# Performance work log

Measured on AMD Instinct MI355X. Metric: run time of the kernel, lower is better.

The kernel has to match this reference:

```python
import jax, jax.numpy as jnp
import numpy as np

B, T, E, H = 2, 4096, 768, 12
D = E // H  # head_dim = 64


def setup_inputs() -> dict:
    key = jax.random.key(0)
    ks = jax.random.split(key, 9)
    s = 1.0 / np.sqrt(E)
    return {
        "x": jax.random.normal(ks[0], (B, T, E), dtype=jnp.float32),
        "wq": jax.random.normal(ks[1], (E, E), dtype=jnp.float32) * s,
        "bq": jnp.zeros((E,), dtype=jnp.float32),
        "wk": jax.random.normal(ks[2], (E, E), dtype=jnp.float32) * s,
        "bk": jnp.zeros((E,), dtype=jnp.float32),
        "wv": jax.random.normal(ks[3], (E, E), dtype=jnp.float32) * s,
        "bv": jnp.zeros((E,), dtype=jnp.float32),
        "wo": jax.random.normal(ks[4], (E, E), dtype=jnp.float32) * s,
        "bo": jnp.zeros((E,), dtype=jnp.float32),
    }


def reference(x, wq, bq, wk, bk, wv, bv, wo, bo):
    # Linear projections (torch Linear: x @ W.T + b; weights here stored as (in,out))
    q = x @ wq + bq  # (B,T,E)
    k = x @ wk + bk
    v = x @ wv + bv

    def split(t):
        return t.reshape(B, T, H, D).transpose(0, 2, 1, 3)  # (B,H,T,D)

    q, k, v = split(q), split(k), split(v)
    scale = 1.0 / np.sqrt(D).astype(np.float32)
    scores = jnp.einsum("bhtd,bhsd->bhts", q, k) * scale  # (B,H,T,T)
    causal = jnp.tril(jnp.ones((T, T), dtype=bool))
    scores = jnp.where(causal, scores, -jnp.inf)
    attn = jax.nn.softmax(scores, axis=-1)
    out = jnp.einsum("bhts,bhsd->bhtd", attn, v)  # (B,H,T,D)
    out = out.transpose(0, 2, 1, 3).reshape(B, T, E)
    return out @ wo + bo
```

## Files before the change

### kernel.cpp

```cpp
#include <hip/hip_runtime.h>
#include <hip/hip_bf16.h>

#define TSEQ 4096
#define EMB 768
#define NH 12
#define DH 64
#define BT 8192

typedef __attribute__((ext_vector_type(8))) short bf16x8;
typedef __attribute__((ext_vector_type(4))) float f32x4;

#define FENCE() asm volatile("" ::: "memory")

__device__ __forceinline__ f32x4 mfma16(bf16x8 a, bf16x8 b, f32x4 c) {
    return __builtin_amdgcn_mfma_f32_16x16x32_bf16(a, b, c, 0, 0, 0);
}

__device__ __forceinline__ void gload16(const void* g, void* l) {
    __builtin_amdgcn_global_load_lds((const __attribute__((address_space(1))) void*)g,
                                     (__attribute__((address_space(3))) void*)l, 16, 0, 0);
}

__global__ __launch_bounds__(256) void conv_x_k(const float* __restrict__ x,
                                                __hip_bfloat16* __restrict__ xb) {
    int i = (blockIdx.x * 256 + threadIdx.x) * 4;
    float4 v = *(const float4*)(x + i);
    union { unsigned short u[4]; uint2 p; } o;
    __hip_bfloat16 t0 = __float2bfloat16(v.x); o.u[0] = *(unsigned short*)&t0;
    __hip_bfloat16 t1 = __float2bfloat16(v.y); o.u[1] = *(unsigned short*)&t1;
    __hip_bfloat16 t2 = __float2bfloat16(v.z); o.u[2] = *(unsigned short*)&t2;
    __hip_bfloat16 t3 = __float2bfloat16(v.w); o.u[3] = *(unsigned short*)&t3;
    *(uint2*)(xb + i) = o.p;
}

__global__ __launch_bounds__(256) void conv_w_k(const float* w0, const float* w1,
                                                const float* w2, const float* w3,
                                                __hip_bfloat16* o0, __hip_bfloat16* o1,
                                                __hip_bfloat16* o2, __hip_bfloat16* o3) {
    const float* w; __hip_bfloat16* o;
    switch (blockIdx.z) {
        case 0: w = w0; o = o0; break;
        case 1: w = w1; o = o1; break;
        case 2: w = w2; o = o2; break;
        default: w = w3; o = o3; break;
    }
    __shared__ float tile[32][33];
    int tx = threadIdx.x & 31, ty = threadIdx.x >> 5;
    int kb = blockIdx.y * 32, nb = blockIdx.x * 32;
    for (int i = 0; i < 32; i += 8)
        tile[ty + i][tx] = w[(size_t)(kb + ty + i) * EMB + nb + tx];
    __syncthreads();
    for (int i = 0; i < 32; i += 8)
        o[(size_t)(nb + ty + i) * EMB + kb + tx] = __float2bfloat16(tile[tx][ty + i]);
}

__device__ __forceinline__ void gemm_body(const __hip_bfloat16* __restrict__ A,
                                          const __hip_bfloat16* __restrict__ Wt,
                                          const float* __restrict__ bias,
                                          void* __restrict__ outp, int mode, float scale) {
    __shared__ alignas(16) char As[2][8192];
    __shared__ alignas(16) char Bs[2][8192];
    const int m0 = blockIdx.x * 128, n0 = blockIdx.y * 128;
    const int tid = threadIdx.x;
    const int lane = tid & 63, l15 = lane & 15, lg = lane >> 4;
    const int wave = tid >> 6, wm = wave >> 1, wn = wave & 1;
    const int swz = (l15 & 7) << 4;

    int mrow_[2]; int kelem_[2];
#pragma unroll
    for (int c = 0; c < 2; ++c) {
        int p = c * 4096 + tid * 16;
        int lrow = p >> 7, w = p & 127;
        int wp = w ^ ((lrow & 7) << 4);
        mrow_[c] = lrow + ((wp >> 6) & 1) * 64;
        kelem_[c] = (wp & 63) >> 1;
    }

    f32x4 acc[4][4];
    for (int i = 0; i < 4; ++i)
        for (int j = 0; j < 4; ++j) acc[i][j] = (f32x4){0.f, 0.f, 0.f, 0.f};

    auto stage = [&](int buf, int k0) {
#pragma unroll
        for (int c = 0; c < 2; ++c)
            gload16(A + (size_t)(m0 + mrow_[c]) * EMB + k0 + kelem_[c],
                    As[buf] + c * 4096 + wave * 1024);
#pragma unroll
        for (int c = 0; c < 2; ++c)
            gload16(Wt + (size_t)(n0 + mrow_[c]) * EMB + k0 + kelem_[c],
                    Bs[buf] + c * 4096 + wave * 1024);
    };

    stage(0, 0);
    const int NK = EMB / 32;
    for (int ks = 0; ks < NK; ++ks) {
        const int cur = ks & 1;
        const bool pre = (ks + 1 < NK);
        if (pre) stage(cur ^ 1, (ks + 1) * 32);
        if (pre) asm volatile("s_waitcnt vmcnt(4)" ::: "memory");
        else     asm volatile("s_waitcnt vmcnt(0)" ::: "memory");
        FENCE(); __builtin_amdgcn_s_barrier(); FENCE();
        bf16x8 af[4], bfv[4];
#pragma unroll
        for (int f = 0; f < 4; ++f)
            af[f] = *(const bf16x8*)(As[cur] + (f * 16 + l15) * 128 + ((wm * 64 + lg * 16) ^ swz));
#pragma unroll
        for (int f = 0; f < 4; ++f)
            bfv[f] = *(const bf16x8*)(Bs[cur] + (f * 16 + l15) * 128 + ((wn * 64 + lg * 16) ^ swz));
        __builtin_amdgcn_s_setprio(1);
#pragma unroll
        for (int i = 0; i < 4; ++i)
#pragma unroll
            for (int j = 0; j < 4; ++j)
                acc[i][j] = mfma16(af[i], bfv[j], acc[i][j]);
        __builtin_amdgcn_s_setprio(0);
        FENCE(); __builtin_amdgcn_s_barrier(); FENCE();
    }

#pragma unroll
    for (int i = 0; i < 4; ++i) {
#pragma unroll
        for (int j = 0; j < 4; ++j) {
            const int n = n0 + wn * 64 + j * 16 + l15;
            const float bv = bias[n];
            const int mbase = m0 + wm * 64 + i * 16 + lg * 4;
#pragma unroll
            for (int r = 0; r < 4; ++r) {
                const int m = mbase + r;
                const float val = (acc[i][j][r] + bv) * scale;
                if (mode == 2) {
                    ((float*)outp)[(size_t)m * EMB + n] = val;
                } else {
                    const int b = m >> 12, t = m & (TSEQ - 1);
                    const int h = n >> 6, d = n & 63;
                    size_t addr;
                    if (mode == 0) addr = ((size_t)(b * NH + h) * TSEQ + t) * DH + d;
                    else           addr = ((size_t)(b * NH + h) * DH + d) * TSEQ + t;
                    ((__hip_bfloat16*)outp)[addr] = __float2bfloat16(val);
                }
            }
        }
    }
}

__global__ __launch_bounds__(256) void qkv_k(const __hip_bfloat16* __restrict__ xb,
                                             const __hip_bfloat16* __restrict__ wqT,
                                             const __hip_bfloat16* __restrict__ wkT,
                                             const __hip_bfloat16* __restrict__ wvT,
                                             const float* __restrict__ bq,
                                             const float* __restrict__ bk,
                                             const float* __restrict__ bv,
                                             __hip_bfloat16* __restrict__ qo,
                                             __hip_bfloat16* __restrict__ ko,
                                             __hip_bfloat16* __restrict__ vo) {
    const __hip_bfloat16* Wt; const float* bias; void* o; int mode; float scale;
    const float cq = 0.125f * 1.44269504089f;
    switch (blockIdx.z) {
        case 0:  Wt = wqT; bias = bq; o = qo; mode = 0; scale = cq;  break;
        case 1:  Wt = wkT; bias = bk; o = ko; mode = 0; scale = 1.f; break;
        default: Wt = wvT; bias = bv; o = vo; mode = 1; scale = 1.f; break;
    }
    gemm_body(xb, Wt, bias, o, mode, scale);
}

__global__ __launch_bounds__(256) void oproj_k(const __hip_bfloat16* __restrict__ abf,
                                               const __hip_bfloat16* __restrict__ woT,
                                               const float* __restrict__ bo,
                                               float* __restrict__ out) {
    gemm_body(abf, woT, bo, out, 2, 1.f);
}

__global__ __launch_bounds__(256) void attn_k(const __hip_bfloat16* __restrict__ qb,
                                              const __hip_bfloat16* __restrict__ kb,
                                              const __hip_bfloat16* __restrict__ vt,
                                              __hip_bfloat16* __restrict__ ab) {
    __shared__ alignas(16) char Ks[2][8192];
    __shared__ alignas(16) char Vs[2][8192];
    __shared__ alignas(16) char pbuf[4][2048];
    const int lane = threadIdx.x & 63, l15 = lane & 15, lg = lane >> 4;
    const int wave = threadIdx.x >> 6;
    const int bid = blockIdx.x;
    const int xcd = bid & 7, slot = bid >> 3;
    const int pair = slot & 31, hgrp = slot >> 5;
    const int bh = xcd + hgrp * 8;
    const __hip_bfloat16* Qh = qb + (size_t)bh * TSEQ * DH;
    const __hip_bfloat16* Kh = kb + (size_t)bh * TSEQ * DH;
    const __hip_bfloat16* Vh = vt + (size_t)bh * DH * TSEQ;
    char* Pb = pbuf[wave];
    const int swz = (l15 & 7) << 4;
    const int b = bh / NH, h = bh % NH;

    bf16x8 ones8;
#pragma unroll
    for (int j = 0; j < 8; ++j) ones8[j] = (short)0x3F80;

    unsigned ka[8];
#pragma unroll
    for (int st = 0; st < 4; ++st)
#pragma unroll
        for (int ks = 0; ks < 2; ++ks)
            ka[st * 2 + ks] = (unsigned)((st * 16 + l15) * 128 + ((ks * 64 + lg * 16) ^ swz));
    char* pw[4]; char* pr[2];
#pragma unroll
    for (int st = 0; st < 4; ++st) pw[st] = Pb + l15 * 128 + ((st * 32 + lg * 8) ^ swz);
#pragma unroll
    for (int ks = 0; ks < 2; ++ks) pr[ks] = Pb + l15 * 128 + ((ks * 64 + lg * 16) ^ swz);
    const int dthr = wave * 16 + l15 - lg * 4;

    int r_[2], wp_[2];
#pragma unroll
    for (int c = 0; c < 2; ++c) {
        int p = c * 4096 + wave * 1024 + lane * 16;
        int r = p >> 7, w = p & 127;
        r_[c] = r;
        wp_[c] = (w ^ ((r & 7) << 4)) >> 1;
    }

#define SBODY(BUF, PRE, MASKB) do {                                              \
    if (PRE) {                                                                   \
        gload16(kg0, Ks[(BUF) ^ 1] + wave * 1024);                               \
        gload16(kg1, Ks[(BUF) ^ 1] + 4096 + wave * 1024);                        \
        gload16(vg0, Vs[(BUF) ^ 1] + wave * 1024);                               \
        gload16(vg1, Vs[(BUF) ^ 1] + 4096 + wave * 1024);                        \
        kg0 += 8192; kg1 += 8192; vg0 += 128; vg1 += 128;                        \
        asm volatile("s_waitcnt vmcnt(4)" ::: "memory");                         \
    } else {                                                                     \
        asm volatile("s_waitcnt vmcnt(0)" ::: "memory");                         \
    }                                                                            \
    FENCE(); __builtin_amdgcn_s_barrier(); FENCE();                              \
    f32x4 sa[4];                                                                 \
    __builtin_amdgcn_s_setprio(1);                                               \
    _Pragma("unroll")                                                            \
    for (int st = 0; st < 4; ++st) {                                             \
        f32x4 z = (f32x4){0.f, 0.f, 0.f, 0.f};                                   \
        z = mfma16(*(const bf16x8*)(Ks[BUF] + ka[st * 2 + 0]), qf0, z);          \
        z = mfma16(*(const bf16x8*)(Ks[BUF] + ka[st * 2 + 1]), qf1, z);          \
        sa[st] = z;                                                              \
    }                                                                            \
    __builtin_amdgcn_s_setprio(0);                                               \
    if (MASKB) {                                                                 \
        _Pragma("unroll")                                                        \
        for (int st = 0; st < 4; ++st)                                           \
            _Pragma("unroll")                                                    \
            for (int r = 0; r < 4; ++r)                                          \
                if (st * 16 + r > dthr) sa[st][r] = -INFINITY;                   \
    }                                                                            \
    float mx = fmaxf(fmaxf(sa[0][0], sa[0][1]), sa[0][2]);                       \
    mx = fmaxf(fmaxf(mx, sa[0][3]), sa[1][0]);                                   \
    mx = fmaxf(fmaxf(mx, sa[1][1]), sa[1][2]);                                   \
    mx = fmaxf(fmaxf(mx, sa[1][3]), sa[2][0]);                                   \
    mx = fmaxf(fmaxf(mx, sa[2][1]), sa[2][2]);                                   \
    mx = fmaxf(fmaxf(mx, sa[2][3]), sa[3][0]);                                   \
    mx = fmaxf(fmaxf(mx, sa[3][1]), sa[3][2]);                                   \
    mx = fmaxf(mx, sa[3][3]);                                                    \
    mx = fmaxf(mx, __shfl_xor(mx, 16));                                          \
    mx = fmaxf(mx, __shfl_xor(mx, 32));                                          \
    float mnew = m;                                                              \
    if (!__all(mx <= m + 8.0f)) {                                                \
        mnew = fmaxf(m, mx);                                                     \
        const float rs = exp2f(m - mnew);                                        \
        m = mnew;                                                                \
        float fr[4];                                                             \
        _Pragma("unroll")                                                        \
        for (int r = 0; r < 4; ++r) fr[r] = __shfl(rs, lg * 4 + r);              \
        _Pragma("unroll")                                                        \
        for (int dt = 0; dt < 4; ++dt) {                                         \
            f32x4 ov = o[dt];                                                    \
            _Pragma("unroll")                                                    \
            for (int r = 0; r < 4; ++r) ov[r] *= fr[r];                          \
            o[dt] = ov;                                                          \
        }                                                                        \
        _Pragma("unroll")                                                        \
        for (int r = 0; r < 4; ++r) lacc[r] *= fr[r];                            \
    }                                                                            \
    _Pragma("unroll")                                                            \
    for (int st = 0; st < 4; ++st) {                                             \
        union { unsigned short u[4]; uint2 v; } pk;                              \
        _Pragma("unroll")                                                        \
        for (int r = 0; r < 4; ++r) {                                            \
            const float p = exp2f(sa[st][r] - mnew);                             \
            __hip_bfloat16 hb = __float2bfloat16(p);                             \
            pk.u[r] = *(unsigned short*)&hb;                                     \
        }                                                                        \
        *(uint2*)pw[st] = pk.v;                                                  \
    }                                                                            \
    asm volatile("s_waitcnt lgkmcnt(0)" ::: "memory");                           \
    __builtin_amdgcn_s_setprio(1);                                               \
    bf16x8 pf0 = *(const bf16x8*)pr[0];                                          \
    bf16x8 pf1 = *(const bf16x8*)pr[1];                                          \
    lacc = mfma16(pf0, ones8, lacc);                                             \
    lacc = mfma16(pf1, ones8, lacc);                                             \
    _Pragma("unroll")                                                            \
    for (int dt = 0; dt < 4; ++dt)                                               \
        o[dt] = mfma16(pf0, *(const bf16x8*)(Vs[BUF] + ka[dt * 2 + 0]), o[dt]);  \
    _Pragma("unroll")                                                            \
    for (int dt = 0; dt < 4; ++dt)                                               \
        o[dt] = mfma16(pf1, *(const bf16x8*)(Vs[BUF] + ka[dt * 2 + 1]), o[dt]);  \
    __builtin_amdgcn_s_setprio(0);                                               \
    asm volatile("s_waitcnt lgkmcnt(0)" ::: "memory");                           \
    FENCE(); __builtin_amdgcn_s_barrier(); FENCE();                              \
} while (0)

    for (int tt = 0; tt < 2; ++tt) {
        const int tile = tt ? (63 - pair) : pair;
        const int q0 = tile * 64 + wave * 16;

        bf16x8 qf0 = *(const bf16x8*)(Qh + (size_t)(q0 + l15) * DH + lg * 8);
        bf16x8 qf1 = *(const bf16x8*)(Qh + (size_t)(q0 + l15) * DH + 32 + lg * 8);

        f32x4 o[4];
#pragma unroll
        for (int dt = 0; dt < 4; ++dt) o[dt] = (f32x4){0.f, 0.f, 0.f, 0.f};
        f32x4 lacc = (f32x4){0.f, 0.f, 0.f, 0.f};
        float m = -1e30f;

        const char* kg0 = (const char*)(Kh + (size_t)r_[0] * DH + wp_[0]);
        const char* kg1 = (const char*)(Kh + (size_t)r_[1] * DH + wp_[1]);
        const char* vg0 = (const char*)(Vh + (size_t)r_[0] * TSEQ + wp_[0]);
        const char* vg1 = (const char*)(Vh + (size_t)r_[1] * TSEQ + wp_[1]);

        const int nsb = tile + 1;
        gload16(kg0, Ks[0] + wave * 1024);
        gload16(kg1, Ks[0] + 4096 + wave * 1024);
        gload16(vg0, Vs[0] + wave * 1024);
        gload16(vg1, Vs[0] + 4096 + wave * 1024);
        kg0 += 8192; kg1 += 8192; vg0 += 128; vg1 += 128;

        int sb = 0;
        while (sb + 2 <= nsb) {
            SBODY(0, true, false);
            SBODY(1, (sb + 2 < nsb), (sb + 1 == nsb - 1));
            sb += 2;
        }
        if (sb < nsb) SBODY(0, false, true);

        float inv[4];
#pragma unroll
        for (int r = 0; r < 4; ++r) inv[r] = 1.0f / lacc[r];
#pragma unroll
        for (int r = 0; r < 4; ++r) {
            const int qrow = q0 + lg * 4 + r;
            const size_t rowbase = ((size_t)b * TSEQ + qrow) * EMB + h * DH;
#pragma unroll
            for (int dt = 0; dt < 4; ++dt)
                ab[rowbase + dt * 16 + l15] = __float2bfloat16(o[dt][r] * inv[r]);
        }
    }
#undef SBODY
}

extern "C" void kernel_launch(void* const* d_in, const int* in_sizes, int n_in,
                              void* d_out, int out_size, void* d_ws, size_t ws_size,
                              hipStream_t stream) {
    (void)in_sizes; (void)n_in; (void)out_size; (void)ws_size;
    const float* x  = (const float*)d_in[0];
    const float* wq = (const float*)d_in[1];
    const float* bq = (const float*)d_in[2];
    const float* wk = (const float*)d_in[3];
    const float* bk = (const float*)d_in[4];
    const float* wv = (const float*)d_in[5];
    const float* bv = (const float*)d_in[6];
    const float* wo = (const float*)d_in[7];
    const float* bo = (const float*)d_in[8];
    float* out = (float*)d_out;

    char* ws = (char*)d_ws;
    size_t off = 0;
    auto alloc = [&](size_t bytes) {
        char* p = ws + off;
        off += (bytes + 255) & ~(size_t)255;
        return p;
    };
    __hip_bfloat16* xb  = (__hip_bfloat16*)alloc((size_t)BT * EMB * 2);
    __hip_bfloat16* qbf = (__hip_bfloat16*)alloc((size_t)BT * EMB * 2);
    __hip_bfloat16* kbf = (__hip_bfloat16*)alloc((size_t)BT * EMB * 2);
    __hip_bfloat16* vtb = (__hip_bfloat16*)alloc((size_t)BT * EMB * 2);
    __hip_bfloat16* abf = (__hip_bfloat16*)alloc((size_t)BT * EMB * 2);
    __hip_bfloat16* wqT = (__hip_bfloat16*)alloc((size_t)EMB * EMB * 2);
    __hip_bfloat16* wkT = (__hip_bfloat16*)alloc((size_t)EMB * EMB * 2);
    __hip_bfloat16* wvT = (__hip_bfloat16*)alloc((size_t)EMB * EMB * 2);
    __hip_bfloat16* woT = (__hip_bfloat16*)alloc((size_t)EMB * EMB * 2);

    conv_x_k<<<BT * EMB / 1024, 256, 0, stream>>>(x, xb);
    conv_w_k<<<dim3(24, 24, 4), 256, 0, stream>>>(wq, wk, wv, wo, wqT, wkT, wvT, woT);
    qkv_k<<<dim3(64, 6, 3), 256, 0, stream>>>(xb, wqT, wkT, wvT, bq, bk, bv, qbf, kbf, vtb);
    attn_k<<<768, 256, 0, stream>>>(qbf, kbf, vtb, abf);
    oproj_k<<<dim3(64, 6), 256, 0, stream>>>(abf, woT, bo, out);
}
```

Before: 207.8 us.

## Share K/V tiles between paired causal query tiles in one pass

The attention kernel previously handled its low and high query tiles one after the other, streaming K/V from global memory twice. Now both tiles run in a single pass over K/V: each staged K/V block feeds the high tile and, while still in range, the low tile, so the low tile's global loads are dropped. The load pipeline is reordered so the prefetch is issued after the barrier with a full vmcnt(0) wait, and launch bounds ask for 3 blocks per CU. The cost is higher register pressure from keeping two sets of accumulators and Q fragments, which the occupancy hint may turn into spills. The pipelining is also weaker, since the wait and barrier now come before the prefetch of the next block.

```diff
diff --git a/kernel.cpp b/kernel.cpp
--- a/kernel.cpp
+++ b/kernel.cpp
@@ -170,10 +170,10 @@
     gemm_body(abf, woT, bo, out, 2, 1.f);
 }
 
-__global__ __launch_bounds__(256) void attn_k(const __hip_bfloat16* __restrict__ qb,
-                                              const __hip_bfloat16* __restrict__ kb,
-                                              const __hip_bfloat16* __restrict__ vt,
-                                              __hip_bfloat16* __restrict__ ab) {
+__global__ __launch_bounds__(256, 3) void attn_k(const __hip_bfloat16* __restrict__ qb,
+                                                 const __hip_bfloat16* __restrict__ kb,
+                                                 const __hip_bfloat16* __restrict__ vt,
+                                                 __hip_bfloat16* __restrict__ ab) {
     __shared__ alignas(16) char Ks[2][8192];
     __shared__ alignas(16) char Vs[2][8192];
     __shared__ alignas(16) char pbuf[4][2048];
@@ -216,25 +216,43 @@
         wp_[c] = (w ^ ((r & 7) << 4)) >> 1;
     }
 
-#define SBODY(BUF, PRE, MASKB) do {                                              \
-    if (PRE) {                                                                   \
-        gload16(kg0, Ks[(BUF) ^ 1] + wave * 1024);                               \
-        gload16(kg1, Ks[(BUF) ^ 1] + 4096 + wave * 1024);                        \
-        gload16(vg0, Vs[(BUF) ^ 1] + wave * 1024);                               \
-        gload16(vg1, Vs[(BUF) ^ 1] + 4096 + wave * 1024);                        \
-        kg0 += 8192; kg1 += 8192; vg0 += 128; vg1 += 128;                        \
-        asm volatile("s_waitcnt vmcnt(4)" ::: "memory");                         \
-    } else {                                                                     \
-        asm volatile("s_waitcnt vmcnt(0)" ::: "memory");                         \
-    }                                                                            \
-    FENCE(); __builtin_amdgcn_s_barrier(); FENCE();                              \
+    const int lo = pair, hi = 63 - pair;
+    const int q0l = lo * 64 + wave * 16;
+    const int q0h = hi * 64 + wave * 16;
+    const int nsb = hi + 1;
+
+    bf16x8 qh0 = *(const bf16x8*)(Qh + (size_t)(q0h + l15) * DH + lg * 8);
+    bf16x8 qh1 = *(const bf16x8*)(Qh + (size_t)(q0h + l15) * DH + 32 + lg * 8);
+    bf16x8 ql0 = *(const bf16x8*)(Qh + (size_t)(q0l + l15) * DH + lg * 8);
+    bf16x8 ql1 = *(const bf16x8*)(Qh + (size_t)(q0l + l15) * DH + 32 + lg * 8);
+
+    f32x4 oh[4], ol[4];
+#pragma unroll
+    for (int dt = 0; dt < 4; ++dt) { oh[dt] = (f32x4){0.f,0.f,0.f,0.f}; ol[dt] = (f32x4){0.f,0.f,0.f,0.f}; }
+    f32x4 lh = (f32x4){0.f,0.f,0.f,0.f}, ll = (f32x4){0.f,0.f,0.f,0.f};
+    float mh = -1e30f, ml = -1e30f;
+
+    const char* kg0 = (const char*)(Kh + (size_t)r_[0] * DH + wp_[0]);
+    const char* kg1 = (const char*)(Kh + (size_t)r_[1] * DH + wp_[1]);
+    const char* vg0 = (const char*)(Vh + (size_t)r_[0] * TSEQ + wp_[0]);
+    const char* vg1 = (const char*)(Vh + (size_t)r_[1] * TSEQ + wp_[1]);
+
+#define STAGE(DST) do {                                                          \
+    gload16(kg0, Ks[DST] + wave * 1024);                                         \
+    gload16(kg1, Ks[DST] + 4096 + wave * 1024);                                  \
+    gload16(vg0, Vs[DST] + wave * 1024);                                         \
+    gload16(vg1, Vs[DST] + 4096 + wave * 1024);                                  \
+    kg0 += 8192; kg1 += 8192; vg0 += 128; vg1 += 128;                            \
+} while (0)
+
+#define TUNIT(BUF, Q0, Q1, OV, LA, MM, MASKB) do {                               \
     f32x4 sa[4];                                                                 \
     __builtin_amdgcn_s_setprio(1);                                               \
     _Pragma("unroll")                                                            \
     for (int st = 0; st < 4; ++st) {                                             \
         f32x4 z = (f32x4){0.f, 0.f, 0.f, 0.f};                                   \
-        z = mfma16(*(const bf16x8*)(Ks[BUF] + ka[st * 2 + 0]), qf0, z);          \
-        z = mfma16(*(const bf16x8*)(Ks[BUF] + ka[st * 2 + 1]), qf1, z);          \
+        z = mfma16(*(const bf16x8*)(Ks[BUF] + ka[st * 2 + 0]), Q0, z);           \
+        z = mfma16(*(const bf16x8*)(Ks[BUF] + ka[st * 2 + 1]), Q1, z);           \
         sa[st] = z;                                                              \
     }                                                                            \
     __builtin_amdgcn_s_setprio(0);                                               \
@@ -255,23 +273,23 @@
     mx = fmaxf(mx, sa[3][3]);                                                    \
     mx = fmaxf(mx, __shfl_xor(mx, 16));                                          \
     mx = fmaxf(mx, __shfl_xor(mx, 32));                                          \
-    float mnew = m;                                                              \
-    if (!__all(mx <= m + 8.0f)) {                                                \
-        mnew = fmaxf(m, mx);                                                     \
-        const float rs = exp2f(m - mnew);                                        \
-        m = mnew;                                                                \
+    float mnew = MM;                                                             \
+    if (!__all(mx <= MM + 8.0f)) {                                               \
+        mnew = fmaxf(MM, mx);                                                    \
+        const float rs = exp2f(MM - mnew);                                       \
+        MM = mnew;                                                               \
         float fr[4];                                                             \
         _Pragma("unroll")                                                        \
         for (int r = 0; r < 4; ++r) fr[r] = __shfl(rs, lg * 4 + r);              \
         _Pragma("unroll")                                                        \
         for (int dt = 0; dt < 4; ++dt) {                                         \
-            f32x4 ov = o[dt];                                                    \
+            f32x4 ov = OV[dt];                                                   \
             _Pragma("unroll")                                                    \
             for (int r = 0; r < 4; ++r) ov[r] *= fr[r];                          \
-            o[dt] = ov;                                                          \
+            OV[dt] = ov;                                                         \
         }                                                                        \
         _Pragma("unroll")                                                        \
-        for (int r = 0; r < 4; ++r) lacc[r] *= fr[r];                            \
+        for (int r = 0; r < 4; ++r) LA[r] *= fr[r];                              \
     }                                                                            \
     _Pragma("unroll")                                                            \
     for (int st = 0; st < 4; ++st) {                                             \
@@ -285,68 +303,67 @@
         *(uint2*)pw[st] = pk.v;                                                  \
     }                                                                            \
     asm volatile("s_waitcnt lgkmcnt(0)" ::: "memory");                           \
-    __builtin_amdgcn_s_setprio(1);                                               \
     bf16x8 pf0 = *(const bf16x8*)pr[0];                                          \
     bf16x8 pf1 = *(const bf16x8*)pr[1];                                          \
-    lacc = mfma16(pf0, ones8, lacc);                                             \
-    lacc = mfma16(pf1, ones8, lacc);                                             \
+    __builtin_amdgcn_s_setprio(1);                                               \
+    LA = mfma16(pf0, ones8, LA);                                                 \
+    LA = mfma16(pf1, ones8, LA);                                                 \
     _Pragma("unroll")                                                            \
     for (int dt = 0; dt < 4; ++dt)                                               \
-        o[dt] = mfma16(pf0, *(const bf16x8*)(Vs[BUF] + ka[dt * 2 + 0]), o[dt]);  \
+        OV[dt] = mfma16(pf0, *(const bf16x8*)(Vs[BUF] + ka[dt * 2 + 0]), OV[dt]);\
     _Pragma("unroll")                                                            \
     for (int dt = 0; dt < 4; ++dt)                                               \
-        o[dt] = mfma16(pf1, *(const bf16x8*)(Vs[BUF] + ka[dt * 2 + 1]), o[dt]);  \
+        OV[dt] = mfma16(pf1, *(const bf16x8*)(Vs[BUF] + ka[dt * 2 + 1]), OV[dt]);\
     __builtin_amdgcn_s_setprio(0);                                               \
-    asm volatile("s_waitcnt lgkmcnt(0)" ::: "memory");                           \
+} while (0)
+
+#define SBODY(BUF, PRE, LOACT, MHI, MLO) do {                                    \
+    asm volatile("s_waitcnt vmcnt(0)" ::: "memory");                             \
     FENCE(); __builtin_amdgcn_s_barrier(); FENCE();                              \
+    if (PRE) STAGE((BUF) ^ 1);                                                   \
+    TUNIT(BUF, qh0, qh1, oh, lh, mh, MHI);                                       \
+    if (LOACT) TUNIT(BUF, ql0, ql1, ol, ll, ml, MLO);                            \
 } while (0)
 
-    for (int tt = 0; tt < 2; ++tt) {
-        const int tile = tt ? (63 - pair) : pair;
-        const int q0 = tile * 64 + wave * 16;
-
-        bf16x8 qf0 = *(const bf16x8*)(Qh + (size_t)(q0 + l15) * DH + lg * 8);
-        bf16x8 qf1 = *(const bf16x8*)(Qh + (size_t)(q0 + l15) * DH + 32 + lg * 8);
-
-        f32x4 o[4];
-#pragma unroll
-        for (int dt = 0; dt < 4; ++dt) o[dt] = (f32x4){0.f, 0.f, 0.f, 0.f};
-        f32x4 lacc = (f32x4){0.f, 0.f, 0.f, 0.f};
-        float m = -1e30f;
-
-        const char* kg0 = (const char*)(Kh + (size_t)r_[0] * DH + wp_[0]);
-        const char* kg1 = (const char*)(Kh + (size_t)r_[1] * DH + wp_[1]);
-        const char* vg0 = (const char*)(Vh + (size_t)r_[0] * TSEQ + wp_[0]);
-        const char* vg1 = (const char*)(Vh + (size_t)r_[1] * TSEQ + wp_[1]);
-
-        const int nsb = tile + 1;
-        gload16(kg0, Ks[0] + wave * 1024);
-        gload16(kg1, Ks[0] + 4096 + wave * 1024);
-        gload16(vg0, Vs[0] + wave * 1024);
-        gload16(vg1, Vs[0] + 4096 + wave * 1024);
-        kg0 += 8192; kg1 += 8192; vg0 += 128; vg1 += 128;
-
-        int sb = 0;
-        while (sb + 2 <= nsb) {
-            SBODY(0, true, false);
-            SBODY(1, (sb + 2 < nsb), (sb + 1 == nsb - 1));
-            sb += 2;
+    STAGE(0);
+    int sb = 0;
+    while (sb + 2 <= nsb) {
+        SBODY(0, true, sb <= lo, false, sb == lo);
+        SBODY(1, sb + 2 < nsb, sb + 1 <= lo, sb + 1 == nsb - 1, sb + 1 == lo);
+        sb += 2;
+    }
+    if (sb < nsb) SBODY(0, false, sb <= lo, true, sb == lo);
+
+#undef SBODY
+#undef TUNIT
+#undef STAGE
+
+    {
+        float inv[4];
+#pragma unroll
+        for (int r = 0; r < 4; ++r) inv[r] = 1.0f / lh[r];
+#pragma unroll
+        for (int r = 0; r < 4; ++r) {
+            const int qrow = q0h + lg * 4 + r;
+            const size_t rowbase = ((size_t)b * TSEQ + qrow) * EMB + h * DH;
+#pragma unroll
+            for (int dt = 0; dt < 4; ++dt)
+                ab[rowbase + dt * 16 + l15] = __float2bfloat16(oh[dt][r] * inv[r]);
         }
-        if (sb < nsb) SBODY(0, false, true);
-
+    }
+    {
         float inv[4];
 #pragma unroll
-        for (int r = 0; r < 4; ++r) inv[r] = 1.0f / lacc[r];
+        for (int r = 0; r < 4; ++r) inv[r] = 1.0f / ll[r];
 #pragma unroll
         for (int r = 0; r < 4; ++r) {
-            const int qrow = q0 + lg * 4 + r;
+            const int qrow = q0l + lg * 4 + r;
             const size_t rowbase = ((size_t)b * TSEQ + qrow) * EMB + h * DH;
 #pragma unroll
             for (int dt = 0; dt < 4; ++dt)
-                ab[rowbase + dt * 16 + l15] = __float2bfloat16(o[dt][r] * inv[r]);
+                ab[rowbase + dt * 16 + l15] = __float2bfloat16(ol[dt][r] * inv[r]);
         }
     }
-#undef SBODY
 }
 
 extern "C" void kernel_launch(void* const* d_in, const int* in_sizes, int n_in,
```

Measured after the change: 198.9 us. 1.04x faster.

## Rework causal attention to 32x32 MFMA tiles with register-resident P

Applied to the files above, without the earlier changes.

Rewrites the attention kernel so each wave handles 32 query rows with 32x32x16 bf16 MFMAs instead of 16x16x32. The softmax probabilities are exchanged between half-waves with lane shuffles rather than written to and re-read from an LDS staging buffer, which removes that buffer and its waits. Each block now processes one 128-row query tile, ordered largest first, instead of a balanced pair of 64-row tiles. The staging wait becomes a full vmcnt(0) before the barrier, which may reduce load/compute overlap, and the larger accumulators raise register pressure.

```diff
diff --git a/kernel.cpp b/kernel.cpp
--- a/kernel.cpp
+++ b/kernel.cpp
@@ -9,11 +9,21 @@
 
 typedef __attribute__((ext_vector_type(8))) short bf16x8;
 typedef __attribute__((ext_vector_type(4))) float f32x4;
+typedef __attribute__((ext_vector_type(16))) float f32x16;
 
 #define FENCE() asm volatile("" ::: "memory")
 
 __device__ __forceinline__ f32x4 mfma16(bf16x8 a, bf16x8 b, f32x4 c) {
     return __builtin_amdgcn_mfma_f32_16x16x32_bf16(a, b, c, 0, 0, 0);
+}
+__device__ __forceinline__ f32x16 mfma32(bf16x8 a, bf16x8 b, f32x16 c) {
+    return __builtin_amdgcn_mfma_f32_32x32x16_bf16(a, b, c, 0, 0, 0);
+}
+__device__ __forceinline__ f32x16 zero16() {
+    f32x16 z;
+#pragma unroll
+    for (int i = 0; i < 16; ++i) z[i] = 0.f;
+    return z;
 }
 
 __device__ __forceinline__ void gload16(const void* g, void* l) {
@@ -176,36 +186,28 @@
                                               __hip_bfloat16* __restrict__ ab) {
     __shared__ alignas(16) char Ks[2][8192];
     __shared__ alignas(16) char Vs[2][8192];
-    __shared__ alignas(16) char pbuf[4][2048];
-    const int lane = threadIdx.x & 63, l15 = lane & 15, lg = lane >> 4;
+    const int lane = threadIdx.x & 63;
+    const int l31 = lane & 31, hiL = lane >> 5;
     const int wave = threadIdx.x >> 6;
     const int bid = blockIdx.x;
     const int xcd = bid & 7, slot = bid >> 3;
-    const int pair = slot & 31, hgrp = slot >> 5;
+    const int t = 31 - (slot & 31);
+    const int hgrp = slot >> 5;
     const int bh = xcd + hgrp * 8;
     const __hip_bfloat16* Qh = qb + (size_t)bh * TSEQ * DH;
     const __hip_bfloat16* Kh = kb + (size_t)bh * TSEQ * DH;
     const __hip_bfloat16* Vh = vt + (size_t)bh * DH * TSEQ;
-    char* Pb = pbuf[wave];
-    const int swz = (l15 & 7) << 4;
     const int b = bh / NH, h = bh % NH;
 
     bf16x8 ones8;
 #pragma unroll
     for (int j = 0; j < 8; ++j) ones8[j] = (short)0x3F80;
 
-    unsigned ka[8];
-#pragma unroll
-    for (int st = 0; st < 4; ++st)
-#pragma unroll
-        for (int ks = 0; ks < 2; ++ks)
-            ka[st * 2 + ks] = (unsigned)((st * 16 + l15) * 128 + ((ks * 64 + lg * 16) ^ swz));
-    char* pw[4]; char* pr[2];
-#pragma unroll
-    for (int st = 0; st < 4; ++st) pw[st] = Pb + l15 * 128 + ((st * 32 + lg * 8) ^ swz);
-#pragma unroll
-    for (int ks = 0; ks < 2; ++ks) pr[ks] = Pb + l15 * 128 + ((ks * 64 + lg * 16) ^ swz);
-    const int dthr = wave * 16 + l15 - lg * 4;
+    const int swzb = (l31 & 7) << 4;
+    int colx[4];
+#pragma unroll
+    for (int c = 0; c < 4; ++c) colx[c] = (c * 32 + hiL * 16) ^ swzb;
+    const int rb0 = l31 * 128, rb1 = (32 + l31) * 128;
 
     int r_[2], wp_[2];
 #pragma unroll
@@ -216,137 +218,137 @@
         wp_[c] = (w ^ ((r & 7) << 4)) >> 1;
     }
 
-#define SBODY(BUF, PRE, MASKB) do {                                              \
-    if (PRE) {                                                                   \
-        gload16(kg0, Ks[(BUF) ^ 1] + wave * 1024);                               \
-        gload16(kg1, Ks[(BUF) ^ 1] + 4096 + wave * 1024);                        \
-        gload16(vg0, Vs[(BUF) ^ 1] + wave * 1024);                               \
-        gload16(vg1, Vs[(BUF) ^ 1] + 4096 + wave * 1024);                        \
-        kg0 += 8192; kg1 += 8192; vg0 += 128; vg1 += 128;                        \
-        asm volatile("s_waitcnt vmcnt(4)" ::: "memory");                         \
-    } else {                                                                     \
-        asm volatile("s_waitcnt vmcnt(0)" ::: "memory");                         \
-    }                                                                            \
-    FENCE(); __builtin_amdgcn_s_barrier(); FENCE();                              \
-    f32x4 sa[4];                                                                 \
+    const int q0w = t * 128 + wave * 32;
+    const int nsb = 2 * t + 2;
+    const int sbd = (q0w + 31) >> 6;
+    const int dthrh = (q0w - 64 * sbd) + l31 - 4 * hiL;
+
+    const __hip_bfloat16* qrow = Qh + (size_t)(q0w + l31) * DH;
+    bf16x8 qf[4];
+#pragma unroll
+    for (int kd = 0; kd < 4; ++kd)
+        qf[kd] = *(const bf16x8*)(qrow + kd * 16 + hiL * 8);
+
+    f32x16 o0 = zero16(), o1 = zero16(), lacc = zero16();
+    float m = -1e30f;
+
+    const char* kg0 = (const char*)(Kh + (size_t)r_[0] * DH + wp_[0]);
+    const char* kg1 = (const char*)(Kh + (size_t)r_[1] * DH + wp_[1]);
+    const char* vg0 = (const char*)(Vh + (size_t)r_[0] * TSEQ + wp_[0]);
+    const char* vg1 = (const char*)(Vh + (size_t)r_[1] * TSEQ + wp_[1]);
+
+#define STAGE(DST) do {                                                          \
+    gload16(kg0, Ks[DST] + wave * 1024);                                         \
+    gload16(kg1, Ks[DST] + 4096 + wave * 1024);                                  \
+    gload16(vg0, Vs[DST] + wave * 1024);                                         \
+    gload16(vg1, Vs[DST] + 4096 + wave * 1024);                                  \
+    kg0 += 8192; kg1 += 8192; vg0 += 128; vg1 += 128;                            \
+} while (0)
+
+#define TUNIT(BUF, MASKB) do {                                                   \
+    f32x16 a0 = zero16(), a1 = zero16();                                         \
     __builtin_amdgcn_s_setprio(1);                                               \
     _Pragma("unroll")                                                            \
-    for (int st = 0; st < 4; ++st) {                                             \
-        f32x4 z = (f32x4){0.f, 0.f, 0.f, 0.f};                                   \
-        z = mfma16(*(const bf16x8*)(Ks[BUF] + ka[st * 2 + 0]), qf0, z);          \
-        z = mfma16(*(const bf16x8*)(Ks[BUF] + ka[st * 2 + 1]), qf1, z);          \
-        sa[st] = z;                                                              \
+    for (int kd = 0; kd < 4; ++kd) {                                             \
+        a0 = mfma32(*(const bf16x8*)(Ks[BUF] + rb0 + colx[kd]), qf[kd], a0);     \
+        a1 = mfma32(*(const bf16x8*)(Ks[BUF] + rb1 + colx[kd]), qf[kd], a1);     \
     }                                                                            \
     __builtin_amdgcn_s_setprio(0);                                               \
     if (MASKB) {                                                                 \
         _Pragma("unroll")                                                        \
-        for (int st = 0; st < 4; ++st)                                           \
-            _Pragma("unroll")                                                    \
-            for (int r = 0; r < 4; ++r)                                          \
-                if (st * 16 + r > dthr) sa[st][r] = -INFINITY;                   \
-    }                                                                            \
-    float mx = fmaxf(fmaxf(sa[0][0], sa[0][1]), sa[0][2]);                       \
-    mx = fmaxf(fmaxf(mx, sa[0][3]), sa[1][0]);                                   \
-    mx = fmaxf(fmaxf(mx, sa[1][1]), sa[1][2]);                                   \
-    mx = fmaxf(fmaxf(mx, sa[1][3]), sa[2][0]);                                   \
-    mx = fmaxf(fmaxf(mx, sa[2][1]), sa[2][2]);                                   \
-    mx = fmaxf(fmaxf(mx, sa[2][3]), sa[3][0]);                                   \
-    mx = fmaxf(fmaxf(mx, sa[3][1]), sa[3][2]);                                   \
-    mx = fmaxf(mx, sa[3][3]);                                                    \
-    mx = fmaxf(mx, __shfl_xor(mx, 16));                                          \
+        for (int r = 0; r < 16; ++r) {                                           \
+            if ((r & 3) + 8 * (r >> 2) > dthrh) a0[r] = -INFINITY;               \
+            if (32 + (r & 3) + 8 * (r >> 2) > dthrh) a1[r] = -INFINITY;          \
+        }                                                                        \
+    }                                                                            \
+    float mx = a0[0];                                                            \
+    _Pragma("unroll")                                                            \
+    for (int r = 1; r < 16; ++r) mx = fmaxf(mx, a0[r]);                          \
+    _Pragma("unroll")                                                            \
+    for (int r = 0; r < 16; ++r) mx = fmaxf(mx, a1[r]);                          \
     mx = fmaxf(mx, __shfl_xor(mx, 32));                                          \
     float mnew = m;                                                              \
     if (!__all(mx <= m + 8.0f)) {                                                \
         mnew = fmaxf(m, mx);                                                     \
         const float rs = exp2f(m - mnew);                                        \
         m = mnew;                                                                \
-        float fr[4];                                                             \
         _Pragma("unroll")                                                        \
-        for (int r = 0; r < 4; ++r) fr[r] = __shfl(rs, lg * 4 + r);              \
+        for (int r = 0; r < 16; ++r) {                                           \
+            const float fr = __shfl(rs, (r & 3) + 8 * (r >> 2) + 4 * hiL);       \
+            lacc[r] *= fr; o0[r] *= fr; o1[r] *= fr;                             \
+        }                                                                        \
+    }                                                                            \
+    _Pragma("unroll")                                                            \
+    for (int r = 0; r < 16; ++r) {                                               \
+        a0[r] = exp2f(a0[r] - mnew);                                             \
+        a1[r] = exp2f(a1[r] - mnew);                                             \
+    }                                                                            \
+    unsigned uu[2][4][2];                                                        \
+    _Pragma("unroll")                                                            \
+    for (int rg = 0; rg < 4; ++rg) {                                             \
+        asm("v_cvt_pk_bf16_f32 %0, %1, %2" : "=v"(uu[0][rg][0]) : "v"(a0[4*rg+0]), "v"(a0[4*rg+1])); \
+        asm("v_cvt_pk_bf16_f32 %0, %1, %2" : "=v"(uu[0][rg][1]) : "v"(a0[4*rg+2]), "v"(a0[4*rg+3])); \
+        asm("v_cvt_pk_bf16_f32 %0, %1, %2" : "=v"(uu[1][rg][0]) : "v"(a1[4*rg+0]), "v"(a1[4*rg+1])); \
+        asm("v_cvt_pk_bf16_f32 %0, %1, %2" : "=v"(uu[1][rg][1]) : "v"(a1[4*rg+2]), "v"(a1[4*rg+3])); \
+    }                                                                            \
+    unsigned px[2][4][2];                                                        \
+    _Pragma("unroll")                                                            \
+    for (int sp = 0; sp < 2; ++sp)                                               \
         _Pragma("unroll")                                                        \
-        for (int dt = 0; dt < 4; ++dt) {                                         \
-            f32x4 ov = o[dt];                                                    \
-            _Pragma("unroll")                                                    \
-            for (int r = 0; r < 4; ++r) ov[r] *= fr[r];                          \
-            o[dt] = ov;                                                          \
+        for (int rg = 0; rg < 4; ++rg) {                                         \
+            px[sp][rg][0] = __shfl_xor(uu[sp][rg][0], 32);                       \
+            px[sp][rg][1] = __shfl_xor(uu[sp][rg][1], 32);                       \
         }                                                                        \
-        _Pragma("unroll")                                                        \
-        for (int r = 0; r < 4; ++r) lacc[r] *= fr[r];                            \
-    }                                                                            \
-    _Pragma("unroll")                                                            \
-    for (int st = 0; st < 4; ++st) {                                             \
-        union { unsigned short u[4]; uint2 v; } pk;                              \
-        _Pragma("unroll")                                                        \
-        for (int r = 0; r < 4; ++r) {                                            \
-            const float p = exp2f(sa[st][r] - mnew);                             \
-            __hip_bfloat16 hb = __float2bfloat16(p);                             \
-            pk.u[r] = *(unsigned short*)&hb;                                     \
-        }                                                                        \
-        *(uint2*)pw[st] = pk.v;                                                  \
-    }                                                                            \
-    asm volatile("s_waitcnt lgkmcnt(0)" ::: "memory");                           \
+    bf16x8 pf[4];                                                                \
+    _Pragma("unroll")                                                            \
+    for (int c = 0; c < 4; ++c) {                                                \
+        const int sp = c >> 1, rgp = (c & 1) * 2;                                \
+        union { unsigned w[4]; bf16x8 v; } pk_;                                  \
+        pk_.w[0] = hiL ? px[sp][rgp + 1][0] : uu[sp][rgp][0];                    \
+        pk_.w[1] = hiL ? px[sp][rgp + 1][1] : uu[sp][rgp][1];                    \
+        pk_.w[2] = hiL ? uu[sp][rgp + 1][0] : px[sp][rgp][0];                    \
+        pk_.w[3] = hiL ? uu[sp][rgp + 1][1] : px[sp][rgp][1];                    \
+        pf[c] = pk_.v;                                                           \
+    }                                                                            \
     __builtin_amdgcn_s_setprio(1);                                               \
-    bf16x8 pf0 = *(const bf16x8*)pr[0];                                          \
-    bf16x8 pf1 = *(const bf16x8*)pr[1];                                          \
-    lacc = mfma16(pf0, ones8, lacc);                                             \
-    lacc = mfma16(pf1, ones8, lacc);                                             \
-    _Pragma("unroll")                                                            \
-    for (int dt = 0; dt < 4; ++dt)                                               \
-        o[dt] = mfma16(pf0, *(const bf16x8*)(Vs[BUF] + ka[dt * 2 + 0]), o[dt]);  \
-    _Pragma("unroll")                                                            \
-    for (int dt = 0; dt < 4; ++dt)                                               \
-        o[dt] = mfma16(pf1, *(const bf16x8*)(Vs[BUF] + ka[dt * 2 + 1]), o[dt]);  \
+    _Pragma("unroll")                                                            \
+    for (int c = 0; c < 4; ++c) lacc = mfma32(pf[c], ones8, lacc);               \
+    _Pragma("unroll")                                                            \
+    for (int c = 0; c < 4; ++c)                                                  \
+        o0 = mfma32(pf[c], *(const bf16x8*)(Vs[BUF] + rb0 + colx[c]), o0);       \
+    _Pragma("unroll")                                                            \
+    for (int c = 0; c < 4; ++c)                                                  \
+        o1 = mfma32(pf[c], *(const bf16x8*)(Vs[BUF] + rb1 + colx[c]), o1);       \
     __builtin_amdgcn_s_setprio(0);                                               \
-    asm volatile("s_waitcnt lgkmcnt(0)" ::: "memory");                           \
+} while (0)
+
+#define SBODY(BUF, PRE, SBv) do {                                                \
+    asm volatile("s_waitcnt vmcnt(0)" ::: "memory");                             \
     FENCE(); __builtin_amdgcn_s_barrier(); FENCE();                              \
+    if (PRE) STAGE((BUF) ^ 1);                                                   \
+    if ((SBv) <= sbd) TUNIT(BUF, ((SBv) == sbd));                                \
 } while (0)
 
-    for (int tt = 0; tt < 2; ++tt) {
-        const int tile = tt ? (63 - pair) : pair;
-        const int q0 = tile * 64 + wave * 16;
-
-        bf16x8 qf0 = *(const bf16x8*)(Qh + (size_t)(q0 + l15) * DH + lg * 8);
-        bf16x8 qf1 = *(const bf16x8*)(Qh + (size_t)(q0 + l15) * DH + 32 + lg * 8);
-
-        f32x4 o[4];
-#pragma unroll
-        for (int dt = 0; dt < 4; ++dt) o[dt] = (f32x4){0.f, 0.f, 0.f, 0.f};
-        f32x4 lacc = (f32x4){0.f, 0.f, 0.f, 0.f};
-        float m = -1e30f;
-
-        const char* kg0 = (const char*)(Kh + (size_t)r_[0] * DH + wp_[0]);
-        const char* kg1 = (const char*)(Kh + (size_t)r_[1] * DH + wp_[1]);
-        const char* vg0 = (const char*)(Vh + (size_t)r_[0] * TSEQ + wp_[0]);
-        const char* vg1 = (const char*)(Vh + (size_t)r_[1] * TSEQ + wp_[1]);
-
-        const int nsb = tile + 1;
-        gload16(kg0, Ks[0] + wave * 1024);
-        gload16(kg1, Ks[0] + 4096 + wave * 1024);
-        gload16(vg0, Vs[0] + wave * 1024);
-        gload16(vg1, Vs[0] + 4096 + wave * 1024);
-        kg0 += 8192; kg1 += 8192; vg0 += 128; vg1 += 128;
-
-        int sb = 0;
-        while (sb + 2 <= nsb) {
-            SBODY(0, true, false);
-            SBODY(1, (sb + 2 < nsb), (sb + 1 == nsb - 1));
-            sb += 2;
-        }
-        if (sb < nsb) SBODY(0, false, true);
-
-        float inv[4];
-#pragma unroll
-        for (int r = 0; r < 4; ++r) inv[r] = 1.0f / lacc[r];
-#pragma unroll
-        for (int r = 0; r < 4; ++r) {
-            const int qrow = q0 + lg * 4 + r;
-            const size_t rowbase = ((size_t)b * TSEQ + qrow) * EMB + h * DH;
-#pragma unroll
-            for (int dt = 0; dt < 4; ++dt)
-                ab[rowbase + dt * 16 + l15] = __float2bfloat16(o[dt][r] * inv[r]);
-        }
-    }
+    STAGE(0);
+    int sb = 0;
+    while (sb + 2 <= nsb) {
+        SBODY(0, true, sb);
+        SBODY(1, sb + 2 < nsb, sb + 1);
+        sb += 2;
+    }
+
 #undef SBODY
+#undef TUNIT
+#undef STAGE
+
+#pragma unroll
+    for (int r = 0; r < 16; ++r) {
+        const float inv = 1.0f / lacc[r];
+        const int q = q0w + (r & 3) + 8 * (r >> 2) + 4 * hiL;
+        const size_t base = ((size_t)b * TSEQ + q) * EMB + h * DH + l31;
+        ab[base] = __float2bfloat16(o0[r] * inv);
+        ab[base + 32] = __float2bfloat16(o1[r] * inv);
+    }
 }
 
 extern "C" void kernel_launch(void* const* d_in, const int* in_sizes, int n_in,
```

Result: slower. 249.6 us (+20.1%).
